# Performance work log

Hardware: AMD Instinct MI355X
Metric: run time of the kernel (lower is better)

## Reference

```python
import jax, jax.numpy as jnp
import numpy as np

B, N, IN_DIM, OUT_DIM, H = 8, 1024, 256, 256, 4
HD = OUT_DIM // H  # head_dim = 64
NEG = -1e9
EPS = 1e-5


def setup_inputs() -> dict:
    key = jax.random.key(0)
    ks = jax.random.split(key, 9)
    h = jax.random.normal(ks[0], (B, N, IN_DIM), dtype=jnp.float32)
    adj = jax.random.randint(ks[1], (N, N), 0, 2, dtype=jnp.int32)
    adj = adj.at[jnp.arange(N), jnp.arange(N)].set(1)  # self loops so no empty rows
    s = 1.0 / np.sqrt(IN_DIM)
    W = jax.random.uniform(ks[2], (H, IN_DIM, HD), jnp.float32, -s, s)
    sa = 1.0 / np.sqrt(2 * HD)
    a1 = jax.random.uniform(ks[3], (H, HD), jnp.float32, -sa, sa)
    a2 = jax.random.uniform(ks[4], (H, HD), jnp.float32, -sa, sa)
    sp = 1.0 / np.sqrt(OUT_DIM)
    proj_w = jax.random.uniform(ks[5], (OUT_DIM, OUT_DIM), jnp.float32, -sp, sp)
    proj_b = jax.random.uniform(ks[6], (OUT_DIM,), jnp.float32, -sp, sp)
    gamma = jnp.ones((OUT_DIM,), jnp.float32)
    beta = jnp.zeros((OUT_DIM,), jnp.float32)
    return {"h": h, "adj": adj, "W": W, "a1": a1, "a2": a2,
            "proj_w": proj_w, "proj_b": proj_b, "gamma": gamma, "beta": beta}


def reference(h, adj, W, a1, a2, proj_w, proj_b, gamma, beta):
    # Wh: [B,H,N,HD]
    Wh = jnp.einsum('bni,hid->bhnd', h, W)
    # Decompose a([Wh_i || Wh_j]) = a1.Wh_i + a2.Wh_j (same math as concat+linear)
    si = jnp.einsum('bhnd,hd->bhn', Wh, a1)  # [B,H,N]
    sj = jnp.einsum('bhnd,hd->bhn', Wh, a2)
    e = jax.nn.leaky_relu(si[:, :, :, None] + sj[:, :, None, :], 0.2)  # [B,H,N,N]
    mask = (adj == 0)  # [N,N]
    e = jnp.where(mask[None, None], NEG, e)
    alpha = jax.nn.softmax(e, axis=-1)
    out = jnp.einsum('bhnm,bhmd->bhnd', alpha, Wh)  # [B,H,N,HD]
    h_multi = out.transpose(0, 2, 1, 3).reshape(B, N, OUT_DIM)  # concat heads
    h_out = jnp.einsum('bnd,od->bno', h_multi, proj_w) + proj_b
    h_out = h_out + h  # residual (in_dim == out_dim)
    mu = jnp.mean(h_out, axis=-1, keepdims=True)
    var = jnp.mean(jnp.square(h_out - mu), axis=-1, keepdims=True)
    return (h_out - mu) * jax.lax.rsqrt(var + EPS) * gamma + beta
```

## Files before the change

kernel.cpp:

```cpp
#include <hip/hip_runtime.h>
#include <hip/hip_bf16.h>

#define NN 1024
#define LOG2E 1.44269504088896f

typedef __attribute__((ext_vector_type(8))) short short8;
typedef __attribute__((ext_vector_type(4))) float floatx4;
typedef __attribute__((ext_vector_type(4))) int intx4;
typedef __attribute__((ext_vector_type(2))) int intx2;

#define WAIT_VM0()   asm volatile("s_waitcnt vmcnt(0)" ::: "memory")
#define WAIT_LGKM0() asm volatile("s_waitcnt lgkmcnt(0)" ::: "memory")

static __device__ __forceinline__ unsigned pk2(float f0, float f1) {
    unsigned u0 = __float_as_uint(f0) + 0x8000u;
    unsigned u1 = __float_as_uint(f1) + 0x8000u;
    return __builtin_amdgcn_perm(u1, u0, 0x07060302u);
}
static __device__ __forceinline__ short8 pk8(floatx4 v0, floatx4 v1) {
    union { intx4 i; short8 s; } u;
    u.i[0] = (int)pk2(v0[0], v0[1]); u.i[1] = (int)pk2(v0[2], v0[3]);
    u.i[2] = (int)pk2(v1[0], v1[1]); u.i[3] = (int)pk2(v1[2], v1[3]);
    return u.s;
}
static __device__ __forceinline__ void load_lds16(const void* gsrc, void* lds) {
    __builtin_amdgcn_global_load_lds(
        (const __attribute__((address_space(1))) void*)gsrc,
        (__attribute__((address_space(3))) void*)lds, 16, 0, 0);
}

__global__ __launch_bounds__(256) void prep_kernel(
    const float* __restrict__ W, const float* __restrict__ proj_w,
    const int* __restrict__ adj,
    __hip_bfloat16* __restrict__ WTb,
    __hip_bfloat16* __restrict__ pwb,
    unsigned* __restrict__ adjm)
{
    int blk = blockIdx.x, t = threadIdx.x;
    if (blk < 16) {
        int o = blk * 16 + (t >> 4);
        int hh = o >> 6, d = o & 63;
        #pragma unroll
        for (int kk = 0; kk < 16; ++kk) {
            int k = (t & 15) + 16 * kk;
            WTb[(size_t)o * 256 + k] = __float2bfloat16(W[((size_t)hh * 256 + k) * 64 + d]);
        }
    } else if (blk < 32) {
        size_t base = (size_t)(blk - 16) * 4096 + (size_t)t * 16;
        #pragma unroll
        for (int k = 0; k < 16; k += 8) {
            floatx4 v0 = *(const floatx4*)(proj_w + base + k);
            floatx4 v1 = *(const floatx4*)(proj_w + base + k + 4);
            *(short8*)(pwb + base + k) = pk8(v0, v1);
        }
    } else {
        int n = (blk - 32) * 8 + (t >> 5);
        int wd = t & 31;
        const int* arow = adj + (size_t)n * NN + wd * 32;
        unsigned bits = 0;
        #pragma unroll
        for (int j4 = 0; j4 < 8; ++j4) {
            intx4 v = *(const intx4*)(arow + j4 * 4);
            #pragma unroll
            for (int j = 0; j < 4; ++j) if (v[j] != 0) bits |= (1u << (j4 * 4 + j));
        }
        adjm[(size_t)n * 32 + wd] = bits;
    }
}

__global__ __launch_bounds__(256) void wh_kernel(
    const float* __restrict__ h,
    const __hip_bfloat16* __restrict__ WTb,
    const float* __restrict__ a1, const float* __restrict__ a2,
    __hip_bfloat16* __restrict__ WhT,
    float* __restrict__ si, float* __restrict__ sj)
{
    int t = threadIdx.x;
    int w = t >> 6, l = t & 63;
    int rl = l & 15, q = l >> 4;
    int r0 = blockIdx.x * 16;
    int bb = r0 >> 10, n0 = r0 & 1023;

    __shared__ __align__(16) __hip_bfloat16 bst[4][4096];
    __shared__ float redsi[4][4][16];
    __shared__ float redsj[4][4][16];

    short8 af[8];
    const float* Arow = h + (size_t)(r0 + rl) * 256 + q * 8;
    #pragma unroll
    for (int k0 = 0; k0 < 8; ++k0) {
        floatx4 v0 = *(const floatx4*)(Arow + k0 * 32);
        floatx4 v1 = *(const floatx4*)(Arow + k0 * 32 + 4);
        af[k0] = pk8(v0, v1);
    }

    #pragma unroll
    for (int k = 0; k < 8; ++k) {
        int row = k * 2 + (l >> 5);
        int g = (l & 31) ^ (row & 7);
        load_lds16(WTb + (size_t)w * 4096 + row * 256 + g * 8, &bst[w][k * 512]);
    }

    #pragma unroll
    for (int j = 0; j < 4; ++j) {
        WAIT_VM0();
        floatx4 acc = {0.f, 0.f, 0.f, 0.f};
        #pragma unroll
        for (int k0 = 0; k0 < 8; ++k0) {
            int p = ((k0 << 2) + q) ^ (rl & 7);
            short8 bf = *(const short8*)(&bst[w][rl * 256 + p * 8]);
            acc = __builtin_amdgcn_mfma_f32_16x16x32_bf16(af[k0], bf, acc, 0, 0, 0);
        }
        WAIT_LGKM0();
        if (j < 3) {
            int ctn = w + 4 * (j + 1);
            #pragma unroll
            for (int k = 0; k < 8; ++k) {
                int row = k * 2 + (l >> 5);
                int g = (l & 31) ^ (row & 7);
                load_lds16(WTb + (size_t)ctn * 4096 + row * 256 + g * 8, &bst[w][k * 512]);
            }
        }

        intx2 pr;
        pr[0] = (int)pk2(acc[0], acc[1]);
        pr[1] = (int)pk2(acc[2], acc[3]);
        *(intx2*)(WhT + ((size_t)(bb * 4 + j) * 64 + w * 16 + rl) * NN + n0 + q * 4) = pr;

        float av1 = a1[j * 64 + w * 16 + rl] * LOG2E;
        float av2 = a2[j * 64 + w * 16 + rl] * LOG2E;
        #pragma unroll
        for (int i = 0; i < 4; ++i) {
            float p1 = acc[i] * av1, p2 = acc[i] * av2;
            #pragma unroll
            for (int off = 1; off < 16; off <<= 1) {
                p1 += __shfl_xor(p1, off, 64);
                p2 += __shfl_xor(p2, off, 64);
            }
            if (rl == 0) { redsi[w][j][q * 4 + i] = p1; redsj[w][j][q * 4 + i] = p2; }
        }
    }
    __syncthreads();

    if (t < 64) {
        int head = t >> 4, row = t & 15;
        si[(size_t)(bb * 4 + head) * NN + n0 + row] =
            redsi[0][head][row] + redsi[1][head][row] + redsi[2][head][row] + redsi[3][head][row];
    } else if (t < 128) {
        int u = t - 64;
        int head = u >> 4, row = u & 15;
        sj[(size_t)(bb * 4 + head) * NN + n0 + row] =
            redsj[0][head][row] + redsj[1][head][row] + redsj[2][head][row] + redsj[3][head][row];
    }
}

__global__ __launch_bounds__(256) void attn_proj_kernel(
    const unsigned* __restrict__ adjm,
    const __hip_bfloat16* __restrict__ WhT,
    const float* __restrict__ si, const float* __restrict__ sj,
    const __hip_bfloat16* __restrict__ pwb,
    const float* __restrict__ h,
    const float* __restrict__ proj_b, const float* __restrict__ gamma,
    const float* __restrict__ beta,
    float* __restrict__ out)
{
    __shared__ __align__(16) char smem[42752];
    auto bst   = reinterpret_cast<__hip_bfloat16 (*)[4096]>(smem);
    auto pl    = reinterpret_cast<__hip_bfloat16 (*)[16][72]>(smem + 32768);
    auto rinvs = reinterpret_cast<float (*)[16]>(smem + 41984);
    auto pbst  = reinterpret_cast<__hip_bfloat16 (*)[4096]>(smem);
    auto hm    = reinterpret_cast<__hip_bfloat16 (*)[264]>(smem + 32768);
    auto red   = reinterpret_cast<float (*)[4][16]>(smem + 42240);

    int bx = blockIdx.x, t = threadIdx.x;
    int w = t >> 6, l = t & 63;
    int rl = l & 15, q = l >> 4;
    int b = bx >> 6, n0 = (bx & 63) * 16;
    int bh = b * 4 + w;
    int r0 = bx * 16;

    int r = l >> 2, cg = l & 3;
    float sii = si[(size_t)bh * NN + n0 + r];
    const float* sjr = sj + (size_t)bh * NN;
    const unsigned* amrow = adjm + (size_t)(n0 + r) * 32;

    float lsum = 0.f;
    floatx4 acc[4] = { {0,0,0,0}, {0,0,0,0}, {0,0,0,0}, {0,0,0,0} };

    const __hip_bfloat16* Bhead = WhT + (size_t)bh * 64 * NN;
    int lrow = l >> 3;
    int lgrp = (l & 7) ^ lrow;

    for (int it = 0; it < 16; ++it) {
        int m0 = it * 64;
        #pragma unroll
        for (int k = 0; k < 8; ++k)
            load_lds16(Bhead + (size_t)(k * 8 + lrow) * NN + m0 + lgrp * 8, &bst[w][k * 512]);
        {
            int mb = m0 + cg * 16;
            unsigned bits = amrow[(m0 >> 5) + (cg >> 1)] >> ((cg & 1) * 16);
            #pragma unroll
            for (int c4 = 0; c4 < 4; ++c4) {
                floatx4 s4 = *(const floatx4*)(sjr + mb + c4 * 4);
                float pv[4];
                #pragma unroll
                for (int k = 0; k < 4; ++k) {
                    float x = sii + s4[k];
                    x = fmaxf(x, 0.2f * x);
                    x = ((bits >> (c4 * 4 + k)) & 1u) ? x : -1e9f;
                    pv[k] = exp2f(x);
                    lsum += pv[k];
                }
                intx2 two;
                two[0] = (int)pk2(pv[0], pv[1]);
                two[1] = (int)pk2(pv[2], pv[3]);
                *(intx2*)(&pl[w][r][cg * 16 + c4 * 4]) = two;
            }
        }
        WAIT_VM0();
        #pragma unroll
        for (int ks = 0; ks < 2; ++ks) {
            short8 afr = *(const short8*)(&pl[w][rl][ks * 32 + q * 8]);
            #pragma unroll
            for (int dt = 0; dt < 4; ++dt) {
                int p = ((ks << 2) + q) ^ (rl & 7);
                short8 bfr = *(const short8*)(&bst[w][(dt * 16 + rl) * 64 + p * 8]);
                acc[dt] = __builtin_amdgcn_mfma_f32_16x16x32_bf16(afr, bfr, acc[dt], 0, 0, 0);
            }
        }
        WAIT_LGKM0();
    }

    lsum += __shfl_xor(lsum, 1, 64);
    lsum += __shfl_xor(lsum, 2, 64);
    if (cg == 0) rinvs[w][r] = 1.f / lsum;
    float riv[4];
    #pragma unroll
    for (int i = 0; i < 4; ++i) riv[i] = rinvs[w][q * 4 + i];

    #pragma unroll
    for (int k = 0; k < 8; ++k) {
        int row = k * 2 + (l >> 5);
        int g = (l & 31) ^ (row & 7);
        load_lds16(pwb + (size_t)w * 4096 + row * 256 + g * 8, &pbst[w][k * 512]);
    }

    __syncthreads();
    #pragma unroll
    for (int dt = 0; dt < 4; ++dt) {
        #pragma unroll
        for (int i = 0; i < 4; ++i) {
            unsigned uv = (__float_as_uint(acc[dt][i] * riv[i]) + 0x8000u) >> 16;
            hm[q * 4 + i][w * 64 + dt * 16 + rl] = __ushort_as_bfloat16((unsigned short)uv);
        }
    }
    __syncthreads();

    short8 paf[8];
    #pragma unroll
    for (int k0 = 0; k0 < 8; ++k0) paf[k0] = *(const short8*)(&hm[rl][q * 8 + k0 * 32]);

    floatx4 pacc[4];
    #pragma unroll
    for (int j = 0; j < 4; ++j) {
        WAIT_VM0();
        floatx4 a = {0.f, 0.f, 0.f, 0.f};
        #pragma unroll
        for (int k0 = 0; k0 < 8; ++k0) {
            int p = ((k0 << 2) + q) ^ (rl & 7);
            short8 bf = *(const short8*)(&pbst[w][rl * 256 + p * 8]);
            a = __builtin_amdgcn_mfma_f32_16x16x32_bf16(paf[k0], bf, a, 0, 0, 0);
        }
        pacc[j] = a;
        WAIT_LGKM0();
        if (j < 3) {
            int ctn = w + 4 * (j + 1);
            #pragma unroll
            for (int k = 0; k < 8; ++k) {
                int row = k * 2 + (l >> 5);
                int g = (l & 31) ^ (row & 7);
                load_lds16(pwb + (size_t)ctn * 4096 + row * 256 + g * 8, &pbst[w][k * 512]);
            }
        }
    }

    float ps[4] = {0.f, 0.f, 0.f, 0.f};
    #pragma unroll
    for (int j = 0; j < 4; ++j) {
        int col = (w + j * 4) * 16 + rl;
        float pb = proj_b[col];
        #pragma unroll
        for (int i = 0; i < 4; ++i) {
            float v = pacc[j][i] + pb + h[(size_t)(r0 + q * 4 + i) * 256 + col];
            pacc[j][i] = v;
            ps[i] += v;
        }
    }
    #pragma unroll
    for (int i = 0; i < 4; ++i) {
        float s = ps[i];
        #pragma unroll
        for (int off = 1; off < 16; off <<= 1) s += __shfl_xor(s, off, 64);
        ps[i] = s;
    }
    if (rl == 0) {
        for (int i = 0; i < 4; ++i) red[0][w][q * 4 + i] = ps[i];
    }
    __syncthreads();
    float mu[4];
    #pragma unroll
    for (int i = 0; i < 4; ++i) {
        int row = q * 4 + i;
        mu[i] = (red[0][0][row] + red[0][1][row] + red[0][2][row] + red[0][3][row]) * (1.f / 256.f);
    }
    float vs[4] = {0.f, 0.f, 0.f, 0.f};
    #pragma unroll
    for (int j = 0; j < 4; ++j) {
        #pragma unroll
        for (int i = 0; i < 4; ++i) { float cv = pacc[j][i] - mu[i]; vs[i] += cv * cv; }
    }
    #pragma unroll
    for (int i = 0; i < 4; ++i) {
        float s = vs[i];
        #pragma unroll
        for (int off = 1; off < 16; off <<= 1) s += __shfl_xor(s, off, 64);
        vs[i] = s;
    }
    if (rl == 0) {
        for (int i = 0; i < 4; ++i) red[1][w][q * 4 + i] = vs[i];
    }
    __syncthreads();
    float rs[4];
    #pragma unroll
    for (int i = 0; i < 4; ++i) {
        int row = q * 4 + i;
        float var = (red[1][0][row] + red[1][1][row] + red[1][2][row] + red[1][3][row]) * (1.f / 256.f);
        rs[i] = rsqrtf(var + 1e-5f);
    }
    #pragma unroll
    for (int j = 0; j < 4; ++j) {
        int col = (w + j * 4) * 16 + rl;
        float g = gamma[col], be = beta[col];
        #pragma unroll
        for (int i = 0; i < 4; ++i)
            out[(size_t)(r0 + q * 4 + i) * 256 + col] = (pacc[j][i] - mu[i]) * rs[i] * g + be;
    }
}

extern "C" void kernel_launch(void* const* d_in, const int* in_sizes, int n_in,
                              void* d_out, int out_size, void* d_ws, size_t ws_size,
                              hipStream_t stream) {
    const float* h      = (const float*)d_in[0];
    const int*   adj    = (const int*)d_in[1];
    const float* W      = (const float*)d_in[2];
    const float* a1     = (const float*)d_in[3];
    const float* a2     = (const float*)d_in[4];
    const float* proj_w = (const float*)d_in[5];
    const float* proj_b = (const float*)d_in[6];
    const float* gamma  = (const float*)d_in[7];
    const float* beta   = (const float*)d_in[8];
    float* out = (float*)d_out;

    char* ws = (char*)d_ws;
    __hip_bfloat16* WhT = (__hip_bfloat16*)ws;   ws += (size_t)32 * 64 * NN * 2;
    __hip_bfloat16* WTb = (__hip_bfloat16*)ws;   ws += 256 * 256 * 2;
    __hip_bfloat16* pwb = (__hip_bfloat16*)ws;   ws += 256 * 256 * 2;
    float* si = (float*)ws;                      ws += (size_t)32 * NN * 4;
    float* sj = (float*)ws;                      ws += (size_t)32 * NN * 4;
    unsigned* adjm = (unsigned*)ws;              ws += (size_t)NN * 32 * 4;

    prep_kernel<<<160, 256, 0, stream>>>(W, proj_w, adj, WTb, pwb, adjm);
    wh_kernel<<<512, 256, 0, stream>>>(h, WTb, a1, a2, WhT, si, sj);
    attn_proj_kernel<<<512, 256, 0, stream>>>(adjm, WhT, si, sj, pwb, h, proj_b, gamma, beta, out);
}
```

Before: 120.3 us.

## Double-buffer WhT tiles in the attention loop to prefetch the next tile

The per-iteration global-to-LDS load of the Wh^T tile now goes into a two-slot buffer. The next tile is issued before the current scores are computed, so the copy can overlap the score math and the MFMA work instead of stalling each iteration. A partial vmcnt(8) wait replaces the full drain inside the loop, and the final tile is peeled out of the loop. LDS per block grows to about 75 KB, which may lower the number of resident blocks. The in-order vmcnt counter mixed with the sj loads may also limit how much the loads actually overlap.

```diff
diff --git a/kernel.cpp b/kernel.cpp
--- a/kernel.cpp
+++ b/kernel.cpp
@@ -10,6 +10,7 @@
 typedef __attribute__((ext_vector_type(2))) int intx2;
 
 #define WAIT_VM0()   asm volatile("s_waitcnt vmcnt(0)" ::: "memory")
+#define WAIT_VM8()   asm volatile("s_waitcnt vmcnt(8)" ::: "memory")
 #define WAIT_LGKM0() asm volatile("s_waitcnt lgkmcnt(0)" ::: "memory")
 
 static __device__ __forceinline__ unsigned pk2(float f0, float f1) {
@@ -164,13 +165,12 @@
     const float* __restrict__ beta,
     float* __restrict__ out)
 {
-    __shared__ __align__(16) char smem[42752];
-    auto bst   = reinterpret_cast<__hip_bfloat16 (*)[4096]>(smem);
-    auto pl    = reinterpret_cast<__hip_bfloat16 (*)[16][72]>(smem + 32768);
-    auto rinvs = reinterpret_cast<float (*)[16]>(smem + 41984);
-    auto pbst  = reinterpret_cast<__hip_bfloat16 (*)[4096]>(smem);
-    auto hm    = reinterpret_cast<__hip_bfloat16 (*)[264]>(smem + 32768);
-    auto red   = reinterpret_cast<float (*)[4][16]>(smem + 42240);
+    __shared__ __align__(16) char smem[75520];
+    auto bst   = reinterpret_cast<__hip_bfloat16 (*)[2][4096]>(smem);
+    auto pl    = reinterpret_cast<__hip_bfloat16 (*)[16][72]>(smem + 65536);
+    auto rinvs = reinterpret_cast<float (*)[16]>(smem + 74752);
+    auto hm    = reinterpret_cast<__hip_bfloat16 (*)[264]>(smem + 65536);
+    auto red   = reinterpret_cast<float (*)[4][16]>(smem + 75008);
 
     int bx = blockIdx.x, t = threadIdx.x;
     int w = t >> 6, l = t & 63;
@@ -191,45 +191,65 @@
     int lrow = l >> 3;
     int lgrp = (l & 7) ^ lrow;
 
-    for (int it = 0; it < 16; ++it) {
-        int m0 = it * 64;
+    #pragma unroll
+    for (int k = 0; k < 8; ++k)
+        load_lds16(Bhead + (size_t)(k * 8 + lrow) * NN + lgrp * 8, &bst[w][0][k * 512]);
+
+#define SCORES(IT)                                                              \
+    do {                                                                        \
+        int m0_ = (IT) * 64;                                                    \
+        int mb_ = m0_ + cg * 16;                                                \
+        unsigned bits_ = amrow[(m0_ >> 5) + (cg >> 1)] >> ((cg & 1) * 16);      \
+        _Pragma("unroll")                                                       \
+        for (int c4 = 0; c4 < 4; ++c4) {                                        \
+            floatx4 s4_ = *(const floatx4*)(sjr + mb_ + c4 * 4);                \
+            float pv_[4];                                                       \
+            _Pragma("unroll")                                                   \
+            for (int k = 0; k < 4; ++k) {                                       \
+                float x_ = sii + s4_[k];                                        \
+                x_ = fmaxf(x_, 0.2f * x_);                                      \
+                x_ = ((bits_ >> (c4 * 4 + k)) & 1u) ? x_ : -1e9f;               \
+                pv_[k] = exp2f(x_);                                             \
+                lsum += pv_[k];                                                 \
+            }                                                                   \
+            intx2 two_;                                                         \
+            two_[0] = (int)pk2(pv_[0], pv_[1]);                                 \
+            two_[1] = (int)pk2(pv_[2], pv_[3]);                                 \
+            *(intx2*)(&pl[w][r][cg * 16 + c4 * 4]) = two_;                      \
+        }                                                                       \
+    } while (0)
+
+#define MFMA_TILE(CUR)                                                          \
+    do {                                                                        \
+        _Pragma("unroll")                                                       \
+        for (int ks = 0; ks < 2; ++ks) {                                        \
+            short8 afr_ = *(const short8*)(&pl[w][rl][ks * 32 + q * 8]);        \
+            _Pragma("unroll")                                                   \
+            for (int dt = 0; dt < 4; ++dt) {                                    \
+                int p_ = ((ks << 2) + q) ^ (rl & 7);                            \
+                short8 bfr_ = *(const short8*)(&bst[w][CUR][(dt * 16 + rl) * 64 + p_ * 8]); \
+                acc[dt] = __builtin_amdgcn_mfma_f32_16x16x32_bf16(afr_, bfr_, acc[dt], 0, 0, 0); \
+            }                                                                   \
+        }                                                                       \
+    } while (0)
+
+    for (int it = 0; it < 15; ++it) {
+        int cur = it & 1;
+        int m1 = (it + 1) * 64;
         #pragma unroll
         for (int k = 0; k < 8; ++k)
-            load_lds16(Bhead + (size_t)(k * 8 + lrow) * NN + m0 + lgrp * 8, &bst[w][k * 512]);
-        {
-            int mb = m0 + cg * 16;
-            unsigned bits = amrow[(m0 >> 5) + (cg >> 1)] >> ((cg & 1) * 16);
-            #pragma unroll
-            for (int c4 = 0; c4 < 4; ++c4) {
-                floatx4 s4 = *(const floatx4*)(sjr + mb + c4 * 4);
-                float pv[4];
-                #pragma unroll
-                for (int k = 0; k < 4; ++k) {
-                    float x = sii + s4[k];
-                    x = fmaxf(x, 0.2f * x);
-                    x = ((bits >> (c4 * 4 + k)) & 1u) ? x : -1e9f;
-                    pv[k] = exp2f(x);
-                    lsum += pv[k];
-                }
-                intx2 two;
-                two[0] = (int)pk2(pv[0], pv[1]);
-                two[1] = (int)pk2(pv[2], pv[3]);
-                *(intx2*)(&pl[w][r][cg * 16 + c4 * 4]) = two;
-            }
-        }
-        WAIT_VM0();
-        #pragma unroll
-        for (int ks = 0; ks < 2; ++ks) {
-            short8 afr = *(const short8*)(&pl[w][rl][ks * 32 + q * 8]);
-            #pragma unroll
-            for (int dt = 0; dt < 4; ++dt) {
-                int p = ((ks << 2) + q) ^ (rl & 7);
-                short8 bfr = *(const short8*)(&bst[w][(dt * 16 + rl) * 64 + p * 8]);
-                acc[dt] = __builtin_amdgcn_mfma_f32_16x16x32_bf16(afr, bfr, acc[dt], 0, 0, 0);
-            }
-        }
-        WAIT_LGKM0();
-    }
+            load_lds16(Bhead + (size_t)(k * 8 + lrow) * NN + m1 + lgrp * 8,
+                       &bst[w][cur ^ 1][k * 512]);
+        SCORES(it);
+        WAIT_VM8();
+        MFMA_TILE(cur);
+    }
+    SCORES(15);
+    WAIT_VM0();
+    MFMA_TILE(1);
+
+#undef SCORES
+#undef MFMA_TILE
 
     lsum += __shfl_xor(lsum, 1, 64);
     lsum += __shfl_xor(lsum, 2, 64);
@@ -238,11 +258,12 @@
     #pragma unroll
     for (int i = 0; i < 4; ++i) riv[i] = rinvs[w][q * 4 + i];
 
+    __hip_bfloat16* pb = &bst[w][0][0];
     #pragma unroll
     for (int k = 0; k < 8; ++k) {
         int row = k * 2 + (l >> 5);
         int g = (l & 31) ^ (row & 7);
-        load_lds16(pwb + (size_t)w * 4096 + row * 256 + g * 8, &pbst[w][k * 512]);
+        load_lds16(pwb + (size_t)w * 4096 + row * 256 + g * 8, pb + k * 512);
     }
 
     __syncthreads();
@@ -268,7 +289,7 @@
         #pragma unroll
         for (int k0 = 0; k0 < 8; ++k0) {
             int p = ((k0 << 2) + q) ^ (rl & 7);
-            short8 bf = *(const short8*)(&pbst[w][rl * 256 + p * 8]);
+            short8 bf = *(const short8*)(pb + rl * 256 + p * 8);
             a = __builtin_amdgcn_mfma_f32_16x16x32_bf16(paf[k0], bf, a, 0, 0, 0);
         }
         pacc[j] = a;
@@ -279,7 +300,7 @@
             for (int k = 0; k < 8; ++k) {
                 int row = k * 2 + (l >> 5);
                 int g = (l & 31) ^ (row & 7);
-                load_lds16(pwb + (size_t)ctn * 4096 + row * 256 + g * 8, &pbst[w][k * 512]);
+                load_lds16(pwb + (size_t)ctn * 4096 + row * 256 + g * 8, pb + k * 512);
             }
         }
     }
@@ -288,10 +309,10 @@
     #pragma unroll
     for (int j = 0; j < 4; ++j) {
         int col = (w + j * 4) * 16 + rl;
-        float pb = proj_b[col];
+        float pbias = proj_b[col];
         #pragma unroll
         for (int i = 0; i < 4; ++i) {
-            float v = pacc[j][i] + pb + h[(size_t)(r0 + q * 4 + i) * 256 + col];
+            float v = pacc[j][i] + pbias + h[(size_t)(r0 + q * 4 + i) * 256 + col];
             pacc[j][i] = v;
             ps[i] += v;
         }
```

Measured after the change: 121.2 us. Within noise of the previous version (+0.8%).
